# Kernel optimization log

Hardware: AMD Instinct MI355X
Metric: run time of the kernel (lower is better)

The kernel has to match this reference:

```python
import jax, jax.numpy as jnp
import numpy as np

SHIFT = 3
SHIFT2 = 1
POOL_K = 9
MAX_LEN = 16384
BATCH = 256


def _avg_pool1d(x, k, s):
    # x: [..., L] -> VALID average pool over last axis
    acc = jax.lax.reduce_window(x, 0.0, jax.lax.add,
                                (1,) * (x.ndim - 1) + (k,),
                                (1,) * (x.ndim - 1) + (s,), 'VALID')
    return acc / k


def _max_pool1d(x, k, s):
    return jax.lax.reduce_window(x, -jnp.inf, jax.lax.max,
                                 (1,) * (x.ndim - 1) + (k,),
                                 (1,) * (x.ndim - 1) + (s,), 'VALID')


def _upsample_nearest(x, size):
    # torch nn.Upsample(mode='nearest') to target length `size`
    m = x.shape[-1]
    idx = (jnp.arange(size) * m) // size
    return x[..., idx]


def setup_inputs() -> dict:
    key = jax.random.key(0)
    x = jax.random.normal(key, (BATCH, MAX_LEN), dtype=jnp.float32)
    return {"x": x}


def reference(x) -> jnp.ndarray:
    # First derivatives: fixed conv [[-1],[1]] over (rolled, original) row pairs
    # is exactly diff_d = x - roll(x, 2^d).  [B, shift, L]
    deriv1 = jnp.stack([x - jnp.roll(x, 1 << d, axis=-1) for d in range(SHIFT)], axis=1)
    # Second derivatives from the first diff channel (deriv1[:, 0]).
    d0 = deriv1[:, 0]
    deriv2 = jnp.stack([d0 - jnp.roll(d0, 1 << d, axis=-1) for d in range(SHIFT2)], axis=1)
    res = jnp.concatenate([deriv1, deriv2], axis=1)  # [B, shift+shift2, L]
    # Crop the wrapped-around prefix.
    off = max(1 << (SHIFT - 1), 1 << (SHIFT2 - 1))
    res = res[:, :, off:]
    # AvgPool1d(kernel=poolKernel, stride=1)
    res = _avg_pool1d(res, POOL_K, 1)  # [B, C, width]
    width = res.shape[-1]
    # MultiScale: four pool+upsample+residual branches, concat on channel dim.
    branches = [
        _upsample_nearest(_avg_pool1d(res, POOL_K, 1), width) + res,
        _upsample_nearest(_avg_pool1d(res, POOL_K, POOL_K), width) + res,
        _upsample_nearest(_max_pool1d(res, POOL_K, 1), width) + res,
        _upsample_nearest(_max_pool1d(res, POOL_K, POOL_K), width) + res,
    ]
    return jnp.concatenate(branches, axis=1)  # [B, 4*C, width]
```

## Files before the change

kernel.cpp:

```cpp
#include <hip/hip_runtime.h>

#define MAX_LEN 16384
#define RES_LEN 16372
#define P2_LEN  1819
#define NG      4093

__global__ __launch_bounds__(512, 4)
void derive_kernel(const float* __restrict__ x, float* __restrict__ out) {
    const int bid = blockIdx.x;
    const int k_  = bid >> 3;
    const int b   = ((bid & 7) << 5) | (k_ >> 2);
    const int c   = k_ & 3;

    const float*  __restrict__ xr  = x + (size_t)b * MAX_LEN;
    const float4* __restrict__ xr4 = (const float4*)xr;

    __shared__ float4 resS4[4096];
    __shared__ float  a2S[P2_LEN + 1];
    __shared__ float  m2S[P2_LEN + 1];
    float* resS = (float*)resS4;

    const float inv9 = 1.0f / 9.0f;
    const int tid = threadIdx.x;

    for (int g = tid; g < NG; g += 512) {
        float4 A = xr4[g], B4 = xr4[g + 1], C4 = xr4[g + 2], D4 = xr4[g + 3];
        float xv[16];
        xv[0]=A.x;  xv[1]=A.y;  xv[2]=A.z;  xv[3]=A.w;
        xv[4]=B4.x; xv[5]=B4.y; xv[6]=B4.z; xv[7]=B4.w;
        xv[8]=C4.x; xv[9]=C4.y; xv[10]=C4.z; xv[11]=C4.w;
        xv[12]=D4.x; xv[13]=D4.y; xv[14]=D4.z; xv[15]=D4.w;
        float rr[4];
        if (c == 0) {
            #pragma unroll
            for (int j = 0; j < 4; ++j) rr[j] = (xv[j+12] - xv[j+3]) * inv9;
        } else if (c == 1) {
            #pragma unroll
            for (int j = 0; j < 4; ++j) rr[j] = ((xv[j+12] + xv[j+11]) - (xv[j+3] + xv[j+2])) * inv9;
        } else if (c == 2) {
            #pragma unroll
            for (int j = 0; j < 4; ++j) rr[j] = ((xv[j+9] + xv[j+10] + xv[j+11] + xv[j+12])
                                               - (xv[j] + xv[j+1] + xv[j+2] + xv[j+3])) * inv9;
        } else {
            #pragma unroll
            for (int j = 0; j < 4; ++j) rr[j] = ((xv[j+12] - xv[j+11]) - (xv[j+3] - xv[j+2])) * inv9;
        }
        float4 rv; rv.x = rr[0]; rv.y = rr[1]; rv.z = rr[2]; rv.w = rr[3];
        resS4[g] = rv;
    }
    __syncthreads();

    for (int p = tid; p < P2_LEN; p += 512) {
        const int j0 = 9 * p;
        float s = resS[j0], m = resS[j0];
        #pragma unroll
        for (int t = 1; t < 9; ++t) { float v = resS[j0 + t]; s += v; m = fmaxf(m, v); }
        a2S[p] = s * inv9; m2S[p] = m;
    }
    __syncthreads();

    float* outBase = out + ((size_t)b * 16 + c) * RES_LEN;
    float4* o0p = (float4*)(outBase);
    float4* o1p = (float4*)(outBase + 4 * RES_LEN);
    float4* o2p = (float4*)(outBase + 8 * RES_LEN);
    float4* o3p = (float4*)(outBase + 12 * RES_LEN);

    for (int g = tid; g < NG; g += 512) {
        const unsigned i0 = 4u * (unsigned)g;
        const unsigned p1_0 = (i0 * 16364u) / 16372u;
        const unsigned p1_1 = ((i0 + 1u) * 16364u) / 16372u;
        const unsigned p1_2 = ((i0 + 2u) * 16364u) / 16372u;
        const unsigned p1_3 = ((i0 + 3u) * 16364u) / 16372u;
        const unsigned p2_0 = (i0 * 1819u) / 16372u;
        const unsigned p2_1 = ((i0 + 1u) * 1819u) / 16372u;
        const unsigned p2_2 = ((i0 + 2u) * 1819u) / 16372u;
        const unsigned p2_3 = ((i0 + 3u) * 1819u) / 16372u;
        const unsigned q  = p1_0 >> 2;
        const unsigned o0 = p1_0 & 3u;
        const unsigned o1 = p1_1 - 4u * q;
        const unsigned o2 = p1_2 - 4u * q;
        const unsigned o3 = p1_3 - 4u * q;

        float4 W0 = resS4[q], W1 = resS4[q + 1], W2 = resS4[q + 2], W3 = resS4[q + 3];
        float w[16];
        w[0]=W0.x;  w[1]=W0.y;  w[2]=W0.z;  w[3]=W0.w;
        w[4]=W1.x;  w[5]=W1.y;  w[6]=W1.z;  w[7]=W1.w;
        w[8]=W2.x;  w[9]=W2.y;  w[10]=W2.z; w[11]=W2.w;
        w[12]=W3.x; w[13]=W3.y; w[14]=W3.z; w[15]=W3.w;

        float s_[7];
        s_[0] = ((((((((w[0] + w[1]) + w[2]) + w[3]) + w[4]) + w[5]) + w[6]) + w[7]) + w[8]);
        #pragma unroll
        for (int e = 1; e < 7; ++e) s_[e] = s_[e - 1] - w[e - 1] + w[e + 8];

        float suf[7];
        suf[6] = fmaxf(fmaxf(w[6], w[7]), w[8]);
        #pragma unroll
        for (int t = 5; t >= 0; --t) suf[t] = fmaxf(w[t], suf[t + 1]);
        float pre[15];
        pre[8] = w[8];
        #pragma unroll
        for (int u = 9; u < 15; ++u) pre[u] = fmaxf(pre[u - 1], w[u]);
        float m_[7];
        #pragma unroll
        for (int o = 0; o < 7; ++o) m_[o] = fmaxf(suf[o], pre[o + 8]);

        float sum0 = s_[0], sum1 = s_[0], sum2 = s_[0], sum3 = s_[0];
        float mx0  = m_[0], mx1  = m_[0], mx2  = m_[0], mx3  = m_[0];
        #pragma unroll
        for (int e = 1; e <= 3; ++e) { bool t_ = (o0 >= (unsigned)e); sum0 = t_ ? s_[e] : sum0; mx0 = t_ ? m_[e] : mx0; }
        #pragma unroll
        for (int e = 1; e <= 4; ++e) { bool t_ = (o1 >= (unsigned)e); sum1 = t_ ? s_[e] : sum1; mx1 = t_ ? m_[e] : mx1; }
        #pragma unroll
        for (int e = 1; e <= 5; ++e) { bool t_ = (o2 >= (unsigned)e); sum2 = t_ ? s_[e] : sum2; mx2 = t_ ? m_[e] : mx2; }
        #pragma unroll
        for (int e = 1; e <= 6; ++e) { bool t_ = (o3 >= (unsigned)e); sum3 = t_ ? s_[e] : sum3; mx3 = t_ ? m_[e] : mx3; }

        const float4 R = resS4[g];

        const float a2l = a2S[p2_0], a2h = a2S[p2_3];
        const float m2l = m2S[p2_0], m2h = m2S[p2_3];
        const float a2_1 = (p2_1 != p2_0) ? a2h : a2l;
        const float a2_2 = (p2_2 != p2_0) ? a2h : a2l;
        const float m2_1 = (p2_1 != p2_0) ? m2h : m2l;
        const float m2_2 = (p2_2 != p2_0) ? m2h : m2l;

        float4 v0, v1, v2, v3;
        v0.x = sum0 * inv9 + R.x; v0.y = sum1 * inv9 + R.y; v0.z = sum2 * inv9 + R.z; v0.w = sum3 * inv9 + R.w;
        v1.x = a2l + R.x;         v1.y = a2_1 + R.y;        v1.z = a2_2 + R.z;        v1.w = a2h + R.w;
        v2.x = mx0 + R.x;         v2.y = mx1 + R.y;         v2.z = mx2 + R.z;         v2.w = mx3 + R.w;
        v3.x = m2l + R.x;         v3.y = m2_1 + R.y;        v3.z = m2_2 + R.z;        v3.w = m2h + R.w;

        o0p[g] = v0; o1p[g] = v1; o2p[g] = v2; o3p[g] = v3;
    }
}

extern "C" void kernel_launch(void* const* d_in, const int* in_sizes, int n_in,
                              void* d_out, int out_size, void* d_ws, size_t ws_size,
                              hipStream_t stream) {
    const float* x = (const float*)d_in[0];
    float* out = (float*)d_out;
    derive_kernel<<<dim3(256 * 4), dim3(512), 0, stream>>>(x, out);
}
```

Before: 62.07 us.

## Specialize waves per output branch and use nontemporal stores

The output phase is split across waves: three waves compute the stride-1 average branch, three compute the stride-1 max branch, and one wave each handles the two stride-9 branches. Each output stream is written with nontemporal float4 stores, and launch bounds are relaxed from 4 to 2 blocks per SM. The intent is to shrink per-thread register pressure and redundant work per loop iteration and to stream output past the cache. The risk is load imbalance between waves, since the stride-9 waves do cheaper work per element but each covers the full range alone, and lower occupancy from the changed launch bounds.

```diff
diff --git a/kernel.cpp b/kernel.cpp
--- a/kernel.cpp
+++ b/kernel.cpp
@@ -5,7 +5,14 @@
 #define P2_LEN  1819
 #define NG      4093
 
-__global__ __launch_bounds__(512, 4)
+typedef float f4 __attribute__((ext_vector_type(4)));
+
+__device__ __forceinline__ void nt_store4(float* p, float a, float b, float c, float d) {
+    f4 v; v.x = a; v.y = b; v.z = c; v.w = d;
+    __builtin_nontemporal_store(v, (f4*)p);
+}
+
+__global__ __launch_bounds__(512, 2)
 void derive_kernel(const float* __restrict__ x, float* __restrict__ out) {
     const int bid = blockIdx.x;
     const int k_  = bid >> 3;
@@ -60,78 +67,133 @@
     __syncthreads();
 
     float* outBase = out + ((size_t)b * 16 + c) * RES_LEN;
-    float4* o0p = (float4*)(outBase);
-    float4* o1p = (float4*)(outBase + 4 * RES_LEN);
-    float4* o2p = (float4*)(outBase + 8 * RES_LEN);
-    float4* o3p = (float4*)(outBase + 12 * RES_LEN);
-
-    for (int g = tid; g < NG; g += 512) {
-        const unsigned i0 = 4u * (unsigned)g;
-        const unsigned p1_0 = (i0 * 16364u) / 16372u;
-        const unsigned p1_1 = ((i0 + 1u) * 16364u) / 16372u;
-        const unsigned p1_2 = ((i0 + 2u) * 16364u) / 16372u;
-        const unsigned p1_3 = ((i0 + 3u) * 16364u) / 16372u;
-        const unsigned p2_0 = (i0 * 1819u) / 16372u;
-        const unsigned p2_1 = ((i0 + 1u) * 1819u) / 16372u;
-        const unsigned p2_2 = ((i0 + 2u) * 1819u) / 16372u;
-        const unsigned p2_3 = ((i0 + 3u) * 1819u) / 16372u;
-        const unsigned q  = p1_0 >> 2;
-        const unsigned o0 = p1_0 & 3u;
-        const unsigned o1 = p1_1 - 4u * q;
-        const unsigned o2 = p1_2 - 4u * q;
-        const unsigned o3 = p1_3 - 4u * q;
-
-        float4 W0 = resS4[q], W1 = resS4[q + 1], W2 = resS4[q + 2], W3 = resS4[q + 3];
-        float w[16];
-        w[0]=W0.x;  w[1]=W0.y;  w[2]=W0.z;  w[3]=W0.w;
-        w[4]=W1.x;  w[5]=W1.y;  w[6]=W1.z;  w[7]=W1.w;
-        w[8]=W2.x;  w[9]=W2.y;  w[10]=W2.z; w[11]=W2.w;
-        w[12]=W3.x; w[13]=W3.y; w[14]=W3.z; w[15]=W3.w;
-
-        float s_[7];
-        s_[0] = ((((((((w[0] + w[1]) + w[2]) + w[3]) + w[4]) + w[5]) + w[6]) + w[7]) + w[8]);
-        #pragma unroll
-        for (int e = 1; e < 7; ++e) s_[e] = s_[e - 1] - w[e - 1] + w[e + 8];
-
-        float suf[7];
-        suf[6] = fmaxf(fmaxf(w[6], w[7]), w[8]);
-        #pragma unroll
-        for (int t = 5; t >= 0; --t) suf[t] = fmaxf(w[t], suf[t + 1]);
-        float pre[15];
-        pre[8] = w[8];
-        #pragma unroll
-        for (int u = 9; u < 15; ++u) pre[u] = fmaxf(pre[u - 1], w[u]);
-        float m_[7];
-        #pragma unroll
-        for (int o = 0; o < 7; ++o) m_[o] = fmaxf(suf[o], pre[o + 8]);
-
-        float sum0 = s_[0], sum1 = s_[0], sum2 = s_[0], sum3 = s_[0];
-        float mx0  = m_[0], mx1  = m_[0], mx2  = m_[0], mx3  = m_[0];
-        #pragma unroll
-        for (int e = 1; e <= 3; ++e) { bool t_ = (o0 >= (unsigned)e); sum0 = t_ ? s_[e] : sum0; mx0 = t_ ? m_[e] : mx0; }
-        #pragma unroll
-        for (int e = 1; e <= 4; ++e) { bool t_ = (o1 >= (unsigned)e); sum1 = t_ ? s_[e] : sum1; mx1 = t_ ? m_[e] : mx1; }
-        #pragma unroll
-        for (int e = 1; e <= 5; ++e) { bool t_ = (o2 >= (unsigned)e); sum2 = t_ ? s_[e] : sum2; mx2 = t_ ? m_[e] : mx2; }
-        #pragma unroll
-        for (int e = 1; e <= 6; ++e) { bool t_ = (o3 >= (unsigned)e); sum3 = t_ ? s_[e] : sum3; mx3 = t_ ? m_[e] : mx3; }
-
-        const float4 R = resS4[g];
-
-        const float a2l = a2S[p2_0], a2h = a2S[p2_3];
-        const float m2l = m2S[p2_0], m2h = m2S[p2_3];
-        const float a2_1 = (p2_1 != p2_0) ? a2h : a2l;
-        const float a2_2 = (p2_2 != p2_0) ? a2h : a2l;
-        const float m2_1 = (p2_1 != p2_0) ? m2h : m2l;
-        const float m2_2 = (p2_2 != p2_0) ? m2h : m2l;
-
-        float4 v0, v1, v2, v3;
-        v0.x = sum0 * inv9 + R.x; v0.y = sum1 * inv9 + R.y; v0.z = sum2 * inv9 + R.z; v0.w = sum3 * inv9 + R.w;
-        v1.x = a2l + R.x;         v1.y = a2_1 + R.y;        v1.z = a2_2 + R.z;        v1.w = a2h + R.w;
-        v2.x = mx0 + R.x;         v2.y = mx1 + R.y;         v2.z = mx2 + R.z;         v2.w = mx3 + R.w;
-        v3.x = m2l + R.x;         v3.y = m2_1 + R.y;        v3.z = m2_2 + R.z;        v3.w = m2h + R.w;
-
-        o0p[g] = v0; o1p[g] = v1; o2p[g] = v2; o3p[g] = v3;
+    const int wid  = tid >> 6;
+    const int lane = tid & 63;
+
+    if (wid < 3) {
+        float* op = outBase;
+        const int g0 = wid * 1365;
+        const int g1 = (wid == 2) ? NG : (g0 + 1365);
+        for (int g = g0 + lane; g < g1; g += 64) {
+            const unsigned i0 = 4u * (unsigned)g;
+            const unsigned p1_0 = (i0 * 16364u) / 16372u;
+            const unsigned p1_1 = ((i0 + 1u) * 16364u) / 16372u;
+            const unsigned p1_2 = ((i0 + 2u) * 16364u) / 16372u;
+            const unsigned p1_3 = ((i0 + 3u) * 16364u) / 16372u;
+            const unsigned q  = p1_0 >> 2;
+            const unsigned o0 = p1_0 & 3u;
+            const unsigned o1 = p1_1 - 4u * q;
+            const unsigned o2 = p1_2 - 4u * q;
+            const unsigned o3 = p1_3 - 4u * q;
+
+            float4 W0 = resS4[q], W1 = resS4[q + 1], W2 = resS4[q + 2], W3 = resS4[q + 3];
+            float w[16];
+            w[0]=W0.x;  w[1]=W0.y;  w[2]=W0.z;  w[3]=W0.w;
+            w[4]=W1.x;  w[5]=W1.y;  w[6]=W1.z;  w[7]=W1.w;
+            w[8]=W2.x;  w[9]=W2.y;  w[10]=W2.z; w[11]=W2.w;
+            w[12]=W3.x; w[13]=W3.y; w[14]=W3.z; w[15]=W3.w;
+
+            float s_[7];
+            s_[0] = ((((((((w[0]+w[1])+w[2])+w[3])+w[4])+w[5])+w[6])+w[7])+w[8]);
+            #pragma unroll
+            for (int e = 1; e < 7; ++e) s_[e] = s_[e-1] - w[e-1] + w[e+8];
+
+            float sum0 = s_[0], sum1 = s_[0], sum2 = s_[0], sum3 = s_[0];
+            #pragma unroll
+            for (int e = 1; e <= 3; ++e) { if (o0 >= (unsigned)e) sum0 = s_[e]; }
+            #pragma unroll
+            for (int e = 1; e <= 4; ++e) { if (o1 >= (unsigned)e) sum1 = s_[e]; }
+            #pragma unroll
+            for (int e = 1; e <= 5; ++e) { if (o2 >= (unsigned)e) sum2 = s_[e]; }
+            #pragma unroll
+            for (int e = 1; e <= 6; ++e) { if (o3 >= (unsigned)e) sum3 = s_[e]; }
+
+            const float4 R = resS4[g];
+            nt_store4(op + 4 * (size_t)g,
+                      sum0 * inv9 + R.x, sum1 * inv9 + R.y,
+                      sum2 * inv9 + R.z, sum3 * inv9 + R.w);
+        }
+    } else if (wid < 6) {
+        float* op = outBase + 8 * RES_LEN;
+        const int g0 = (wid - 3) * 1365;
+        const int g1 = (wid == 5) ? NG : (g0 + 1365);
+        for (int g = g0 + lane; g < g1; g += 64) {
+            const unsigned i0 = 4u * (unsigned)g;
+            const unsigned p1_0 = (i0 * 16364u) / 16372u;
+            const unsigned p1_1 = ((i0 + 1u) * 16364u) / 16372u;
+            const unsigned p1_2 = ((i0 + 2u) * 16364u) / 16372u;
+            const unsigned p1_3 = ((i0 + 3u) * 16364u) / 16372u;
+            const unsigned q  = p1_0 >> 2;
+            const unsigned o0 = p1_0 & 3u;
+            const unsigned o1 = p1_1 - 4u * q;
+            const unsigned o2 = p1_2 - 4u * q;
+            const unsigned o3 = p1_3 - 4u * q;
+
+            float4 W0 = resS4[q], W1 = resS4[q + 1], W2 = resS4[q + 2], W3 = resS4[q + 3];
+            float w[16];
+            w[0]=W0.x;  w[1]=W0.y;  w[2]=W0.z;  w[3]=W0.w;
+            w[4]=W1.x;  w[5]=W1.y;  w[6]=W1.z;  w[7]=W1.w;
+            w[8]=W2.x;  w[9]=W2.y;  w[10]=W2.z; w[11]=W2.w;
+            w[12]=W3.x; w[13]=W3.y; w[14]=W3.z; w[15]=W3.w;
+
+            float suf[7];
+            suf[6] = fmaxf(fmaxf(w[6], w[7]), w[8]);
+            #pragma unroll
+            for (int t = 5; t >= 0; --t) suf[t] = fmaxf(w[t], suf[t + 1]);
+            float pre[15];
+            pre[8] = w[8];
+            #pragma unroll
+            for (int u = 9; u < 15; ++u) pre[u] = fmaxf(pre[u - 1], w[u]);
+            float m_[7];
+            #pragma unroll
+            for (int o = 0; o < 7; ++o) m_[o] = fmaxf(suf[o], pre[o + 8]);
+
+            float mx0 = m_[0], mx1 = m_[0], mx2 = m_[0], mx3 = m_[0];
+            #pragma unroll
+            for (int e = 1; e <= 3; ++e) { if (o0 >= (unsigned)e) mx0 = m_[e]; }
+            #pragma unroll
+            for (int e = 1; e <= 4; ++e) { if (o1 >= (unsigned)e) mx1 = m_[e]; }
+            #pragma unroll
+            for (int e = 1; e <= 5; ++e) { if (o2 >= (unsigned)e) mx2 = m_[e]; }
+            #pragma unroll
+            for (int e = 1; e <= 6; ++e) { if (o3 >= (unsigned)e) mx3 = m_[e]; }
+
+            const float4 R = resS4[g];
+            nt_store4(op + 4 * (size_t)g,
+                      mx0 + R.x, mx1 + R.y, mx2 + R.z, mx3 + R.w);
+        }
+    } else if (wid == 6) {
+        float* op = outBase + 4 * RES_LEN;
+        #pragma unroll 4
+        for (int g = lane; g < NG; g += 64) {
+            const unsigned i0 = 4u * (unsigned)g;
+            const unsigned p2_0 = (i0 * 1819u) / 16372u;
+            const unsigned p2_1 = ((i0 + 1u) * 1819u) / 16372u;
+            const unsigned p2_2 = ((i0 + 2u) * 1819u) / 16372u;
+            const unsigned p2_3 = ((i0 + 3u) * 1819u) / 16372u;
+            const float a2l = a2S[p2_0], a2h = a2S[p2_3];
+            const float a2_1 = (p2_1 != p2_0) ? a2h : a2l;
+            const float a2_2 = (p2_2 != p2_0) ? a2h : a2l;
+            const float4 R = resS4[g];
+            nt_store4(op + 4 * (size_t)g,
+                      a2l + R.x, a2_1 + R.y, a2_2 + R.z, a2h + R.w);
+        }
+    } else {
+        float* op = outBase + 12 * RES_LEN;
+        #pragma unroll 4
+        for (int g = lane; g < NG; g += 64) {
+            const unsigned i0 = 4u * (unsigned)g;
+            const unsigned p2_0 = (i0 * 1819u) / 16372u;
+            const unsigned p2_1 = ((i0 + 1u) * 1819u) / 16372u;
+            const unsigned p2_2 = ((i0 + 2u) * 1819u) / 16372u;
+            const unsigned p2_3 = ((i0 + 3u) * 1819u) / 16372u;
+            const float m2l = m2S[p2_0], m2h = m2S[p2_3];
+            const float m2_1 = (p2_1 != p2_0) ? m2h : m2l;
+            const float m2_2 = (p2_2 != p2_0) ? m2h : m2l;
+            const float4 R = resS4[g];
+            nt_store4(op + 4 * (size_t)g,
+                      m2l + R.x, m2_1 + R.y, m2_2 + R.z, m2h + R.w);
+        }
     }
 }
 
```

Result: slower. 81.32 us (+31.0%).

## Split each row-channel block into four segments with smaller shared tiles

Applied to the files above, without the earlier changes.

Each block now handles one quarter of the output length for a (batch, channel) pair rather than the whole row. It computes only the needed window of res plus halo into a much smaller shared buffer, and builds a local slice of the stride-9 pooled arrays. The grid grows 4x with 256-thread blocks, and the reduced LDS footprint allows far more resident blocks per CU. The cost is redundant halo computation, extra index arithmetic, and a less cache-friendly block-to-batch mapping than the previous interleaved ordering.

```diff
diff --git a/kernel.cpp b/kernel.cpp
--- a/kernel.cpp
+++ b/kernel.cpp
@@ -2,29 +2,47 @@
 
 #define MAX_LEN 16384
 #define RES_LEN 16372
-#define P2_LEN  1819
-#define NG      4093
+#define NSEG    4
+#define SEG     4096
 
-__global__ __launch_bounds__(512, 4)
+__global__ __launch_bounds__(256, 6)
 void derive_kernel(const float* __restrict__ x, float* __restrict__ out) {
     const int bid = blockIdx.x;
-    const int k_  = bid >> 3;
-    const int b   = ((bid & 7) << 5) | (k_ >> 2);
-    const int c   = k_ & 3;
+    const int b = bid >> 4;
+    const int c = (bid >> 2) & 3;
+    const int s = bid & 3;
 
     const float*  __restrict__ xr  = x + (size_t)b * MAX_LEN;
     const float4* __restrict__ xr4 = (const float4*)xr;
 
-    __shared__ float4 resS4[4096];
-    __shared__ float  a2S[P2_LEN + 1];
-    __shared__ float  m2S[P2_LEN + 1];
+    const unsigned i0     = (unsigned)s * SEG;
+    const unsigned i_last = (s == NSEG - 1) ? (RES_LEN - 1) : (i0 + SEG - 1);
+    const int      nq     = (s == NSEG - 1) ? 1021 : 1024;
+    const unsigned p1_i0  = (i0 * 16364u) / 16372u;
+    const unsigned p2_i0  = (i0 * 1819u)  / 16372u;
+    const unsigned p1_lst = (i_last * 16364u) / 16372u;
+    const unsigned p2_lst = (i_last * 1819u)  / 16372u;
+    const unsigned j_lo   = min(p1_i0, 9u * p2_i0);
+    const unsigned j_lo_al = j_lo & ~3u;
+    const unsigned j_hi   = max(p1_lst, 9u * p2_lst) + 8u;
+    const int      nqw    = (int)((j_hi - j_lo_al + 1u + 3u) >> 2);
+    const int      xqb    = (int)(j_lo_al >> 2);
+    const int      np2    = (int)(p2_lst - p2_i0 + 1u);
+
+    __shared__ float4 resS4[1036];
+    __shared__ float  a2S[456];
+    __shared__ float  m2S[456];
     float* resS = (float*)resS4;
 
     const float inv9 = 1.0f / 9.0f;
     const int tid = threadIdx.x;
 
-    for (int g = tid; g < NG; g += 512) {
-        float4 A = xr4[g], B4 = xr4[g + 1], C4 = xr4[g + 2], D4 = xr4[g + 3];
+    for (int g = tid; g < nqw; g += 256) {
+        const int gi = xqb + g;
+        float4 A  = xr4[gi];
+        float4 B4 = xr4[min(gi + 1, 4095)];
+        float4 C4 = xr4[min(gi + 2, 4095)];
+        float4 D4 = xr4[min(gi + 3, 4095)];
         float xv[16];
         xv[0]=A.x;  xv[1]=A.y;  xv[2]=A.z;  xv[3]=A.w;
         xv[4]=B4.x; xv[5]=B4.y; xv[6]=B4.z; xv[7]=B4.w;
@@ -50,12 +68,12 @@
     }
     __syncthreads();
 
-    for (int p = tid; p < P2_LEN; p += 512) {
-        const int j0 = 9 * p;
-        float s = resS[j0], m = resS[j0];
+    for (int t = tid; t < np2; t += 256) {
+        const int j0 = (int)(9u * (p2_i0 + (unsigned)t) - j_lo_al);
+        float sm = resS[j0], mm = resS[j0];
         #pragma unroll
-        for (int t = 1; t < 9; ++t) { float v = resS[j0 + t]; s += v; m = fmaxf(m, v); }
-        a2S[p] = s * inv9; m2S[p] = m;
+        for (int k = 1; k < 9; ++k) { float v = resS[j0 + k]; sm += v; mm = fmaxf(mm, v); }
+        a2S[t] = sm * inv9; m2S[t] = mm;
     }
     __syncthreads();
 
@@ -64,22 +82,26 @@
     float4* o1p = (float4*)(outBase + 4 * RES_LEN);
     float4* o2p = (float4*)(outBase + 8 * RES_LEN);
     float4* o3p = (float4*)(outBase + 12 * RES_LEN);
+    const int gq0 = (int)(i0 >> 2);
 
-    for (int g = tid; g < NG; g += 512) {
-        const unsigned i0 = 4u * (unsigned)g;
-        const unsigned p1_0 = (i0 * 16364u) / 16372u;
-        const unsigned p1_1 = ((i0 + 1u) * 16364u) / 16372u;
-        const unsigned p1_2 = ((i0 + 2u) * 16364u) / 16372u;
-        const unsigned p1_3 = ((i0 + 3u) * 16364u) / 16372u;
-        const unsigned p2_0 = (i0 * 1819u) / 16372u;
-        const unsigned p2_1 = ((i0 + 1u) * 1819u) / 16372u;
-        const unsigned p2_2 = ((i0 + 2u) * 1819u) / 16372u;
-        const unsigned p2_3 = ((i0 + 3u) * 1819u) / 16372u;
-        const unsigned q  = p1_0 >> 2;
-        const unsigned o0 = p1_0 & 3u;
-        const unsigned o1 = p1_1 - 4u * q;
-        const unsigned o2 = p1_2 - 4u * q;
-        const unsigned o3 = p1_3 - 4u * q;
+    for (int t = tid; t < nq; t += 256) {
+        const int gq = gq0 + t;
+        const unsigned iq0 = 4u * (unsigned)gq;
+        const unsigned p1_0 = (iq0 * 16364u) / 16372u;
+        const unsigned p1_1 = ((iq0 + 1u) * 16364u) / 16372u;
+        const unsigned p1_2 = ((iq0 + 2u) * 16364u) / 16372u;
+        const unsigned p1_3 = ((iq0 + 3u) * 16364u) / 16372u;
+        const unsigned p2_0 = (iq0 * 1819u) / 16372u;
+        const unsigned p2_1 = ((iq0 + 1u) * 1819u) / 16372u;
+        const unsigned p2_2 = ((iq0 + 2u) * 1819u) / 16372u;
+        const unsigned p2_3 = ((iq0 + 3u) * 1819u) / 16372u;
+
+        const unsigned li0 = p1_0 - j_lo_al;
+        const unsigned q   = li0 >> 2;
+        const unsigned o0  = li0 & 3u;
+        const unsigned o1  = (p1_1 - j_lo_al) - 4u * q;
+        const unsigned o2  = (p1_2 - j_lo_al) - 4u * q;
+        const unsigned o3  = (p1_3 - j_lo_al) - 4u * q;
 
         float4 W0 = resS4[q], W1 = resS4[q + 1], W2 = resS4[q + 2], W3 = resS4[q + 3];
         float w[16];
@@ -96,7 +118,7 @@
         float suf[7];
         suf[6] = fmaxf(fmaxf(w[6], w[7]), w[8]);
         #pragma unroll
-        for (int t = 5; t >= 0; --t) suf[t] = fmaxf(w[t], suf[t + 1]);
+        for (int u = 5; u >= 0; --u) suf[u] = fmaxf(w[u], suf[u + 1]);
         float pre[15];
         pre[8] = w[8];
         #pragma unroll
@@ -116,10 +138,10 @@
         #pragma unroll
         for (int e = 1; e <= 6; ++e) { bool t_ = (o3 >= (unsigned)e); sum3 = t_ ? s_[e] : sum3; mx3 = t_ ? m_[e] : mx3; }
 
-        const float4 R = resS4[g];
+        const float4 R = resS4[(iq0 - j_lo_al) >> 2];
 
-        const float a2l = a2S[p2_0], a2h = a2S[p2_3];
-        const float m2l = m2S[p2_0], m2h = m2S[p2_3];
+        const float a2l = a2S[p2_0 - p2_i0], a2h = a2S[p2_3 - p2_i0];
+        const float m2l = m2S[p2_0 - p2_i0], m2h = m2S[p2_3 - p2_i0];
         const float a2_1 = (p2_1 != p2_0) ? a2h : a2l;
         const float a2_2 = (p2_2 != p2_0) ? a2h : a2l;
         const float m2_1 = (p2_1 != p2_0) ? m2h : m2l;
@@ -131,7 +153,7 @@
         v2.x = mx0 + R.x;         v2.y = mx1 + R.y;         v2.z = mx2 + R.z;         v2.w = mx3 + R.w;
         v3.x = m2l + R.x;         v3.y = m2_1 + R.y;        v3.z = m2_2 + R.z;        v3.w = m2h + R.w;
 
-        o0p[g] = v0; o1p[g] = v1; o2p[g] = v2; o3p[g] = v3;
+        o0p[gq] = v0; o1p[gq] = v1; o2p[gq] = v2; o3p[gq] = v3;
     }
 }
 
@@ -140,5 +162,5 @@
                               hipStream_t stream) {
     const float* x = (const float*)d_in[0];
     float* out = (float*)d_out;
-    derive_kernel<<<dim3(256 * 4), dim3(512), 0, stream>>>(x, out);
+    derive_kernel<<<dim3(256 * 4 * NSEG), dim3(256), 0, stream>>>(x, out);
 }
```

Result: faster. 57.93 us (-6.7%).
